# Optimization experiments

Measured on AMD Instinct MI355X. Metric: run time of the kernel, lower is better.

Reference implementation:

```python
import jax, jax.numpy as jnp
import numpy as np

I, H, O = 256, 512, 256  # input_size, hidden_size, output_size
B, S = 4096, 50


def _lstm_cell(x_t, h, c, Wih, Whh, bih, bhh):
    # torch gate order: i, f, g, o
    gates = x_t @ Wih.T + h @ Whh.T + bih + bhh  # [B, 4H]
    i, f, g, o = jnp.split(gates, 4, axis=-1)
    i = jax.nn.sigmoid(i)
    f = jax.nn.sigmoid(f)
    g = jnp.tanh(g)
    o = jax.nn.sigmoid(o)
    c_new = f * c + i * g
    h_new = o * jnp.tanh(c_new)
    return h_new, c_new


def setup_inputs() -> dict:
    key = jax.random.key(0)
    ks = jax.random.split(key, 12)
    s_i = 1.0 / np.sqrt(H)  # torch LSTM/Linear init scale
    u = lambda k, shape: jax.random.uniform(k, shape, jnp.float32, -s_i, s_i)
    return {
        "x": jax.random.normal(ks[0], (B, S, I), jnp.float32),
        "enc_Wih": u(ks[1], (4 * H, I)),
        "enc_Whh": u(ks[2], (4 * H, H)),
        "enc_bih": u(ks[3], (4 * H,)),
        "enc_bhh": u(ks[4], (4 * H,)),
        "dec_Wih": u(ks[5], (4 * H, I)),
        "dec_Whh": u(ks[6], (4 * H, H)),
        "dec_bih": u(ks[7], (4 * H,)),
        "dec_bhh": u(ks[8], (4 * H,)),
        "fc_W": u(ks[9], (O, H)),
        "fc_b": u(ks[10], (O,)),
        "target_seq_length": 20,
    }


def reference(x, enc_Wih, enc_Whh, enc_bih, enc_bhh,
              dec_Wih, dec_Whh, dec_bih, dec_bhh,
              fc_W, fc_b, target_seq_length):
    batch = x.shape[0]
    h0 = jnp.zeros((batch, H), x.dtype)
    c0 = jnp.zeros((batch, H), x.dtype)

    # ---- encoder: scan over time ----
    def enc_step(carry, x_t):
        h, c = carry
        h, c = _lstm_cell(x_t, h, c, enc_Wih, enc_Whh, enc_bih, enc_bhh)
        return (h, c), None

    (h, c), _ = jax.lax.scan(enc_step, (h0, c0), jnp.swapaxes(x, 0, 1))

    dec_in0 = jnp.zeros((batch, I), x.dtype)

    def dec_step(carry, _):
        h, c, inp = carry
        h, c = _lstm_cell(inp, h, c, dec_Wih, dec_Whh, dec_bih, dec_bhh)
        out = h @ fc_W.T + fc_b  # [B, O]
        return (h, c, out), out

    _, outs = jax.lax.scan(dec_step, (h, c, dec_in0), None,
                           length=target_seq_length)
    return jnp.swapaxes(outs, 0, 1)  # [B, T, O]
```

## Files before the change

kernel.cpp:

```cpp
#include <hip/hip_runtime.h>

#define I_SZ 256
#define H_SZ 512
#define O_SZ 256
#define B_SZ 4096
#define S_SZ 50
#define T_SZ 20
#define G4H  2048
#define BH   ((size_t)B_SZ * H_SZ)
#define NB   512

#define PAD 72
#define PAD_H 36

typedef _Float16 half8 __attribute__((ext_vector_type(8)));
typedef float f32x4 __attribute__((ext_vector_type(4)));

__device__ __forceinline__ float sigm(float x) {
    return 1.0f / (1.0f + __expf(-x));
}
__device__ __forceinline__ float tanh_fast(float x) {
    float e = __expf(2.0f * x);
    return 1.0f - 2.0f / (e + 1.0f);
}

#define GLDS(gp, lp) __builtin_amdgcn_global_load_lds(                      \
    (const __attribute__((address_space(1))) void*)(gp),                    \
    (__attribute__((address_space(3))) void*)(lp), 16, 0, 0)

#define MEMFENCE asm volatile("" ::: "memory")

__global__ void k_zeroN(unsigned* p, int n) {
    int i = blockIdx.x * blockDim.x + threadIdx.x;
    if (i < n) p[i] = 0u;
}

__global__ void k_cvt(const float* __restrict__ src, _Float16* __restrict__ dst, int n) {
    int i = blockIdx.x * blockDim.x + threadIdx.x;
    if (i < n) dst[i] = (_Float16)src[i];
}

__global__ void k_bias_combine(const float* __restrict__ a, const float* __restrict__ b,
                               float* __restrict__ dst, int n) {
    int i = blockIdx.x * blockDim.x + threadIdx.x;
    if (i < n) dst[i] = a[i] + b[i];
}

__global__ __launch_bounds__(256) void k_cvt_x(const float* __restrict__ x,
                                               _Float16* __restrict__ xT) {
    size_t idx = ((size_t)blockIdx.x * 256 + threadIdx.x) * 8;
    int i = (int)(idx & 255);
    int s = (int)((idx >> 8) % S_SZ);
    size_t b = idx / (256 * S_SZ);
    float4 v0 = *(const float4*)(x + idx);
    float4 v1 = *(const float4*)(x + idx + 4);
    half8 hv;
    hv[0] = (_Float16)v0.x; hv[1] = (_Float16)v0.y;
    hv[2] = (_Float16)v0.z; hv[3] = (_Float16)v0.w;
    hv[4] = (_Float16)v1.x; hv[5] = (_Float16)v1.y;
    hv[6] = (_Float16)v1.z; hv[7] = (_Float16)v1.w;
    *(half8*)(xT + (((size_t)s * B_SZ + b) * I_SZ + i)) = hv;
}

__global__ void k_wenc(const float* __restrict__ eWih, const float* __restrict__ eWhh,
                       _Float16* __restrict__ Wenc) {
    int idx = blockIdx.x * blockDim.x + threadIdx.x;
    int r = idx / 768, col = idx % 768;
    float v = (col < 256) ? eWih[(size_t)r * 256 + col] : eWhh[(size_t)r * 512 + col - 256];
    Wenc[idx] = (_Float16)v;
}

__global__ __launch_bounds__(256) void k_wd(
    const float* __restrict__ dWhh, const float* __restrict__ dWih,
    const float* __restrict__ fcW, _Float16* __restrict__ Wd)
{
    __shared__ float sA[8][256];
    const int tid = threadIdx.x;
    const int r0 = blockIdx.x * 8;
    {
        int linear = tid * 8;
        int row = linear >> 8, col = linear & 255;
        const float4* p = (const float4*)(dWih + (size_t)(r0 + row) * 256 + col);
        float4 v0 = p[0], v1 = p[1];
        *(float4*)&sA[row][col]     = v0;
        *(float4*)&sA[row][col + 4] = v1;
    }
    __syncthreads();
    float acc[8][2] = {};
    const int k = tid;
    for (int i = 0; i < 256; ++i) {
        float w0 = fcW[(size_t)i * 512 + k];
        float w1 = fcW[(size_t)i * 512 + k + 256];
        #pragma unroll
        for (int rr = 0; rr < 8; ++rr) {
            float a = sA[rr][i];
            acc[rr][0] += a * w0;
            acc[rr][1] += a * w1;
        }
    }
    #pragma unroll
    for (int rr = 0; rr < 8; ++rr) {
        size_t base = (size_t)(r0 + rr) * 512;
        Wd[base + k]       = (_Float16)(dWhh[base + k]       + acc[rr][0]);
        Wd[base + k + 256] = (_Float16)(dWhh[base + k + 256] + acc[rr][1]);
    }
}

__global__ __launch_bounds__(256) void k_bd(
    const float* __restrict__ dWih, const float* __restrict__ fcb,
    const float* __restrict__ db, float* __restrict__ bd)
{
    __shared__ float sf[256];
    const int tid = threadIdx.x;
    sf[tid] = fcb[tid];
    __syncthreads();
    int r = blockIdx.x * 256 + tid;
    float acc = db[r];
    const float* row = dWih + (size_t)r * 256;
    for (int o = 0; o < 256; o += 4) {
        float4 v = *(const float4*)(row + o);
        acc += v.x * sf[o] + v.y * sf[o + 1] + v.z * sf[o + 2] + v.w * sf[o + 3];
    }
    bd[r] = acc;
}

__global__ __launch_bounds__(256, 2) void k_lstm_all(
    const _Float16* __restrict__ xT,
    const _Float16* __restrict__ Wenc,
    const _Float16* __restrict__ dWhh_h,
    const _Float16* __restrict__ Wd,
    const float* __restrict__ eb, const float* __restrict__ db,
    const float* __restrict__ bd,
    _Float16* __restrict__ henc,
    _Float16* __restrict__ hseq,
    unsigned* __restrict__ bar)
{
    __shared__ _Float16 lds[2][2][128 * 64];

    const int tid = threadIdx.x;
    const int xcd = blockIdx.x & 7, slot = blockIdx.x >> 3;
    const int mb = xcd * 4 + (slot >> 4);
    const int jb = slot & 15;
    const int m0 = mb * 128, j0 = jb * 32;
    unsigned* grp = bar + mb * 16;

    const int wv = tid >> 6, lane = tid & 63, lrow = lane & 15, lk8 = (lane >> 4) * 8;
    const int wm = wv >> 1, wn = wv & 1;

    const int colb  = (lane & 7) * 16;
    const int scolh = (colb ^ (((lane >> 3) & 7) << 4)) >> 1;
    const _Float16* wEncQ[4]; const _Float16* wD0Q[4]; const _Float16* wDQ[4];
    const _Float16* xQ[4];
    unsigned aOffQ[4];
    int ldsQ[4];
    #pragma unroll
    for (int q = 0; q < 4; ++q) {
        int r = q * 32 + wv * 8 + (lane >> 3);
        int grow = ((r >> 4) & 3) * H_SZ + j0 + (r >> 6) * 16 + (r & 15);
        wEncQ[q] = Wenc   + (size_t)grow * 768 + scolh;
        wD0Q[q]  = dWhh_h + (size_t)grow * 512 + scolh;
        wDQ[q]   = Wd     + (size_t)grow * 512 + scolh;
        xQ[q]    = xT + (size_t)(m0 + r) * I_SZ + scolh;
        aOffQ[q] = (unsigned)((m0 + r) * H_SZ) + scolh;
        ldsQ[q]  = (q * 256 + wv * 64) * 8;
    }

    float ebj[4], dbj[4], bdj[4];
    #pragma unroll
    for (int nf = 0; nf < 4; ++nf) {
        int col = nf * H_SZ + j0 + wn * 16 + lrow;
        ebj[nf] = eb[col]; dbj[nf] = db[col]; bdj[nf] = bd[col];
    }

    float creg[4][4];

    auto wait_group = [&](unsigned target) {
        MEMFENCE;
        if (tid == 0) {
            while (__hip_atomic_load(grp, __ATOMIC_RELAXED, __HIP_MEMORY_SCOPE_AGENT) < target)
                __builtin_amdgcn_s_sleep(1);
        }
        __builtin_amdgcn_s_barrier();
        MEMFENCE;
    };
    auto arrive = [&]() {
        __syncthreads();
        if (tid == 0)
            __hip_atomic_fetch_add(grp, 1u, __ATOMIC_RELAXED, __HIP_MEMORY_SCOPE_AGENT);
    };

    auto compute = [&](int buf, f32x4 (&acc)[4][4]) {
        #pragma unroll
        for (int kc = 0; kc < 2; ++kc) {
            const int sc = (((kc * 32 + lk8) * 2) ^ ((lrow & 7) << 4)) >> 1;
            half8 a[4], b[4];
            #pragma unroll
            for (int mf = 0; mf < 4; ++mf)
                a[mf] = *(const half8*)&lds[buf][0][(wm * 64 + mf * 16 + lrow) * 64 + sc];
            #pragma unroll
            for (int nf = 0; nf < 4; ++nf)
                b[nf] = *(const half8*)&lds[buf][1][(wn * 64 + nf * 16 + lrow) * 64 + sc];
            #pragma unroll
            for (int mf = 0; mf < 4; ++mf)
                #pragma unroll
                for (int nf = 0; nf < 4; ++nf)
                    acc[mf][nf] = __builtin_amdgcn_mfma_f32_16x16x32_f16(a[mf], b[nf], acc[mf][nf], 0, 0, 0);
        }
    };

    auto epilogue = [&](f32x4 (&acc)[4][4], const float (&bj)[4], _Float16* hout, bool first) {
        _Float16* hsm = &lds[0][0][0];
        const int lc = wn * 16 + lrow;
        #pragma unroll
        for (int mf = 0; mf < 4; ++mf)
            #pragma unroll
            for (int r = 0; r < 4; ++r) {
                int lr = wm * 64 + mf * 16 + (lane >> 4) * 4 + r;
                float gi = acc[mf][0][r] + bj[0];
                float gf = acc[mf][1][r] + bj[1];
                float gg = acc[mf][2][r] + bj[2];
                float go = acc[mf][3][r] + bj[3];
                float cold = first ? 0.0f : creg[mf][r];
                float cn = sigm(gf) * cold + sigm(gi) * tanh_fast(gg);
                creg[mf][r] = cn;
                hsm[lr * PAD_H + lc] = (_Float16)(sigm(go) * tanh_fast(cn));
            }
        __syncthreads();
        int rr = tid >> 3, k = tid & 7;
        #pragma unroll
        for (int q = 0; q < 4; ++q) {
            int r = rr + q * 32;
            unsigned long long v = *(const unsigned long long*)&hsm[r * PAD_H + k * 4];
            unsigned long long* dst =
                (unsigned long long*)(hout + (size_t)(m0 + r) * H_SZ + j0) + k;
            __hip_atomic_store(dst, v, __ATOMIC_RELAXED, __HIP_MEMORY_SCOPE_AGENT);
        }
    };

    {
        f32x4 acc[4][4] = {};
        #pragma unroll
        for (int q = 0; q < 4; ++q) { GLDS(xQ[q], &lds[0][0][ldsQ[q]]); GLDS(wEncQ[q], &lds[0][1][ldsQ[q]]); }
        #pragma unroll
        for (int it = 0; it < 4; ++it) {
            if (it < 3) {
                #pragma unroll
                for (int q = 0; q < 4; ++q) {
                    GLDS(xQ[q] + (it + 1) * 64, &lds[(it + 1) & 1][0][ldsQ[q]]);
                    GLDS(wEncQ[q] + (it + 1) * 64, &lds[(it + 1) & 1][1][ldsQ[q]]);
                }
                asm volatile("s_waitcnt vmcnt(8)" ::: "memory");
            } else {
                asm volatile("s_waitcnt vmcnt(0)" ::: "memory");
            }
            __builtin_amdgcn_s_barrier(); MEMFENCE;
            compute(it & 1, acc);
            MEMFENCE; __builtin_amdgcn_s_barrier(); MEMFENCE;
        }
        epilogue(acc, ebj, henc, true);
        arrive();
    }

    for (int s = 1; s < S_SZ; ++s) {
        const size_t xoff = (size_t)s * B_SZ * I_SZ;
        const _Float16* hin = henc + (size_t)(s - 1) * BH;
        _Float16* hout = (s == S_SZ - 1) ? hseq : henc + (size_t)s * BH;
        f32x4 acc[4][4] = {};
        #pragma unroll
        for (int q = 0; q < 4; ++q) { GLDS(xQ[q] + xoff, &lds[0][0][ldsQ[q]]); GLDS(wEncQ[q], &lds[0][1][ldsQ[q]]); }
        #pragma unroll
        for (int it = 0; it < 12; ++it) {
            if (it < 11) {
                if (it == 3) wait_group((unsigned)s * 16u);
                #pragma unroll
                for (int q = 0; q < 4; ++q) {
                    if (it + 1 < 4) GLDS(xQ[q] + xoff + (it + 1) * 64, &lds[(it + 1) & 1][0][ldsQ[q]]);
                    else            GLDS(hin + aOffQ[q] + (it - 3) * 64, &lds[(it + 1) & 1][0][ldsQ[q]]);
                    GLDS(wEncQ[q] + (it + 1) * 64, &lds[(it + 1) & 1][1][ldsQ[q]]);
                }
                asm volatile("s_waitcnt vmcnt(8)" ::: "memory");
            } else {
                asm volatile("s_waitcnt vmcnt(0)" ::: "memory");
            }
            __builtin_amdgcn_s_barrier(); MEMFENCE;
            compute(it & 1, acc);
            MEMFENCE; __builtin_amdgcn_s_barrier(); MEMFENCE;
        }
        epilogue(acc, ebj, hout, false);
        arrive();
    }

    for (int t = 0; t < T_SZ; ++t) {
        const _Float16* hin = hseq + (size_t)t * BH;
        _Float16* hout = hseq + (size_t)(t + 1) * BH;
        const _Float16* wq[4];
        float bj[4];
        #pragma unroll
        for (int q = 0; q < 4; ++q) wq[q] = t ? wDQ[q] : wD0Q[q];
        #pragma unroll
        for (int nf = 0; nf < 4; ++nf) bj[nf] = t ? bdj[nf] : dbj[nf];

        wait_group((unsigned)(S_SZ + t) * 16u);
        f32x4 acc[4][4] = {};
        #pragma unroll
        for (int q = 0; q < 4; ++q) { GLDS(hin + aOffQ[q], &lds[0][0][ldsQ[q]]); GLDS(wq[q], &lds[0][1][ldsQ[q]]); }
        #pragma unroll
        for (int it = 0; it < 8; ++it) {
            if (it < 7) {
                #pragma unroll
                for (int q = 0; q < 4; ++q) {
                    GLDS(hin + aOffQ[q] + (it + 1) * 64, &lds[(it + 1) & 1][0][ldsQ[q]]);
                    GLDS(wq[q] + (it + 1) * 64, &lds[(it + 1) & 1][1][ldsQ[q]]);
                }
                asm volatile("s_waitcnt vmcnt(8)" ::: "memory");
            } else {
                asm volatile("s_waitcnt vmcnt(0)" ::: "memory");
            }
            __builtin_amdgcn_s_barrier(); MEMFENCE;
            compute(it & 1, acc);
            MEMFENCE; __builtin_amdgcn_s_barrier(); MEMFENCE;
        }
        epilogue(acc, bj, hout, false);
        if (t != T_SZ - 1) arrive();
    }
}

__global__ __launch_bounds__(256) void k_fc(
    const _Float16* __restrict__ hseq1,
    const _Float16* __restrict__ W,
    const float* __restrict__ bias,
    float* __restrict__ out)
{
    __shared__ _Float16 Asm[128][PAD];
    __shared__ _Float16 Bsm[128][PAD];

    const int tid = threadIdx.x;
    const int m0 = blockIdx.x * 128;
    const int t  = blockIdx.y;
    const int n0 = blockIdx.z * 128;
    const int wv = tid >> 6, lane = tid & 63, lrow = lane & 15, lk = (lane >> 4) * 8;
    const int wm = wv >> 1, wn = wv & 1;

    f32x4 acc[4][4] = {};

    const int srow = tid >> 3, skc = (tid & 7) * 8;
    const _Float16* A = hseq1 + (size_t)t * BH;

    for (int k0 = 0; k0 < H_SZ; k0 += 64) {
        __syncthreads();
        #pragma unroll
        for (int q = 0; q < 4; ++q) {
            int r = srow + q * 32;
            *(half8*)&Asm[r][skc] = *(const half8*)(A + (size_t)(m0 + r) * H_SZ + k0 + skc);
        }
        #pragma unroll
        for (int q = 0; q < 4; ++q) {
            int rr = srow + q * 32;
            *(half8*)&Bsm[rr][skc] = *(const half8*)(W + (size_t)(n0 + rr) * H_SZ + k0 + skc);
        }
        __syncthreads();
        #pragma unroll
        for (int kc = 0; kc < 64; kc += 32) {
            half8 a[4], b[4];
            #pragma unroll
            for (int mf = 0; mf < 4; ++mf) a[mf] = *(const half8*)&Asm[wm * 64 + mf * 16 + lrow][kc + lk];
            #pragma unroll
            for (int nf = 0; nf < 4; ++nf) b[nf] = *(const half8*)&Bsm[wn * 64 + nf * 16 + lrow][kc + lk];
            #pragma unroll
            for (int mf = 0; mf < 4; ++mf)
                #pragma unroll
                for (int nf = 0; nf < 4; ++nf)
                    acc[mf][nf] = __builtin_amdgcn_mfma_f32_16x16x32_f16(a[mf], b[nf], acc[mf][nf], 0, 0, 0);
        }
    }

    #pragma unroll
    for (int mf = 0; mf < 4; ++mf)
        #pragma unroll
        for (int nf = 0; nf < 4; ++nf) {
            int o = n0 + wn * 64 + nf * 16 + lrow;
            float bv = bias[o];
            #pragma unroll
            for (int r = 0; r < 4; ++r) {
                int m = m0 + wm * 64 + mf * 16 + (lane >> 4) * 4 + r;
                out[(size_t)m * (T_SZ * O_SZ) + (size_t)t * O_SZ + o] = acc[mf][nf][r] + bv;
            }
        }
}

extern "C" void kernel_launch(void* const* d_in, const int* in_sizes, int n_in,
                              void* d_out, int out_size, void* d_ws, size_t ws_size,
                              hipStream_t stream) {
    (void)in_sizes; (void)n_in; (void)out_size; (void)ws_size;

    const float* x    = (const float*)d_in[0];
    const float* eWih = (const float*)d_in[1];
    const float* eWhh = (const float*)d_in[2];
    const float* ebih = (const float*)d_in[3];
    const float* ebhh = (const float*)d_in[4];
    const float* dWih = (const float*)d_in[5];
    const float* dWhh = (const float*)d_in[6];
    const float* dbih = (const float*)d_in[7];
    const float* dbhh = (const float*)d_in[8];
    const float* fcW  = (const float*)d_in[9];
    const float* fcb  = (const float*)d_in[10];
    float* out = (float*)d_out;
    char* ws = (char*)d_ws;

    size_t off = 0;
    auto alloc = [&](size_t bytes) -> void* {
        void* p = ws + off;
        off += (bytes + 255) & ~(size_t)255;
        return p;
    };
    _Float16* xT     = (_Float16*)alloc((size_t)S_SZ * B_SZ * I_SZ * 2);
    _Float16* Wenc   = (_Float16*)alloc((size_t)G4H * (I_SZ + H_SZ) * 2);
    _Float16* dWhh_h = (_Float16*)alloc((size_t)G4H * H_SZ * 2);
    _Float16* Wd     = (_Float16*)alloc((size_t)G4H * H_SZ * 2);
    _Float16* fcW_h  = (_Float16*)alloc((size_t)O_SZ * H_SZ * 2);
    float*    eb     = (float*)alloc(G4H * 4);
    float*    db     = (float*)alloc(G4H * 4);
    float*    bd     = (float*)alloc(G4H * 4);
    _Float16* henc   = (_Float16*)alloc((size_t)(S_SZ - 1) * BH * 2);
    _Float16* hseq   = (_Float16*)alloc((size_t)(T_SZ + 1) * BH * 2);
    unsigned* bar    = (unsigned*)alloc(32 * 16 * 4);

    const int nWhh = G4H * H_SZ;
    const int nFc  = O_SZ * H_SZ;
    const size_t nX = (size_t)B_SZ * S_SZ * I_SZ;

    k_zeroN<<<2, 256, 0, stream>>>(bar, 32 * 16);
    k_cvt_x<<<(int)(nX / 8 / 256), 256, 0, stream>>>(x, xT);
    k_wenc<<<(G4H * 768) / 256, 256, 0, stream>>>(eWih, eWhh, Wenc);
    k_cvt<<<(nWhh + 255) / 256, 256, 0, stream>>>(dWhh, dWhh_h, nWhh);
    k_cvt<<<(nFc + 255) / 256, 256, 0, stream>>>(fcW, fcW_h, nFc);
    k_bias_combine<<<8, 256, 0, stream>>>(ebih, ebhh, eb, G4H);
    k_bias_combine<<<8, 256, 0, stream>>>(dbih, dbhh, db, G4H);
    k_wd<<<256, 256, 0, stream>>>(dWhh, dWih, fcW, Wd);
    k_bd<<<8, 256, 0, stream>>>(dWih, fcb, db, bd);

    k_lstm_all<<<NB, 256, 0, stream>>>(xT, Wenc, dWhh_h, Wd, eb, db, bd,
                                       henc, hseq, bar);

    k_fc<<<dim3(B_SZ / 128, T_SZ, O_SZ / 128), 256, 0, stream>>>(
        hseq + BH, fcW_h, fcb, out);
}
```

Measured before the change: 1.271 ms.

## Load A operand straight to registers and ring-buffer weights in four LDS stages

The recurrent step is restructured so that activation tiles (x and h) are loaded from global memory directly into registers, double-buffered, instead of being staged through LDS. Weight tiles go into a four-slot LDS ring prefetched two iterations ahead, which removes the second block barrier in each K-iteration. The group-arrive signal now fires early in the next step, after its weight loads are issued, so cross-block synchronisation overlaps with prefetch. The cost is more register pressure and less efficient global access for A, and the tighter synchronisation raises the risk of LDS hazards.

```diff
diff --git a/kernel.cpp b/kernel.cpp
--- a/kernel.cpp
+++ b/kernel.cpp
@@ -15,6 +15,8 @@
 
 typedef _Float16 half8 __attribute__((ext_vector_type(8)));
 typedef float f32x4 __attribute__((ext_vector_type(4)));
+
+template<int N> struct IC { static constexpr int value = N; };
 
 __device__ __forceinline__ float sigm(float x) {
     return 1.0f / (1.0f + __expf(-x));
@@ -135,7 +137,7 @@
     _Float16* __restrict__ hseq,
     unsigned* __restrict__ bar)
 {
-    __shared__ _Float16 lds[2][2][128 * 64];
+    __shared__ _Float16 Bs[4][8192];
 
     const int tid = threadIdx.x;
     const int xcd = blockIdx.x & 7, slot = blockIdx.x >> 3;
@@ -147,22 +149,24 @@
     const int wv = tid >> 6, lane = tid & 63, lrow = lane & 15, lk8 = (lane >> 4) * 8;
     const int wm = wv >> 1, wn = wv & 1;
 
-    const int colb  = (lane & 7) * 16;
-    const int scolh = (colb ^ (((lane >> 3) & 7) << 4)) >> 1;
-    const _Float16* wEncQ[4]; const _Float16* wD0Q[4]; const _Float16* wDQ[4];
-    const _Float16* xQ[4];
-    unsigned aOffQ[4];
+    const int scolh = (((lane & 7) * 16) ^ (((lane >> 3) & 7) << 4)) >> 1;
+    unsigned woffE[4], woffD[4];
     int ldsQ[4];
     #pragma unroll
     for (int q = 0; q < 4; ++q) {
         int r = q * 32 + wv * 8 + (lane >> 3);
-        int grow = ((r >> 4) & 3) * H_SZ + j0 + (r >> 6) * 16 + (r & 15);
-        wEncQ[q] = Wenc   + (size_t)grow * 768 + scolh;
-        wD0Q[q]  = dWhh_h + (size_t)grow * 512 + scolh;
-        wDQ[q]   = Wd     + (size_t)grow * 512 + scolh;
-        xQ[q]    = xT + (size_t)(m0 + r) * I_SZ + scolh;
-        aOffQ[q] = (unsigned)((m0 + r) * H_SZ) + scolh;
+        unsigned grow = ((r >> 4) & 3) * H_SZ + j0 + (r >> 6) * 16 + (r & 15);
+        woffE[q] = grow * 768u + scolh;
+        woffD[q] = grow * 512u + scolh;
         ldsQ[q]  = (q * 256 + wv * 64) * 8;
+    }
+
+    unsigned aoffX[4], aoffH[4];
+    #pragma unroll
+    for (int mf = 0; mf < 4; ++mf) {
+        unsigned row = (unsigned)(m0 + wm * 64 + mf * 16 + lrow);
+        aoffX[mf] = row * (unsigned)I_SZ + (unsigned)lk8;
+        aoffH[mf] = row * (unsigned)H_SZ + (unsigned)lk8;
     }
 
     float ebj[4], dbj[4], bdj[4];
@@ -183,33 +187,85 @@
         __builtin_amdgcn_s_barrier();
         MEMFENCE;
     };
-    auto arrive = [&]() {
-        __syncthreads();
-        if (tid == 0)
-            __hip_atomic_fetch_add(grp, 1u, __ATOMIC_RELAXED, __HIP_MEMORY_SCOPE_AGENT);
-    };
-
-    auto compute = [&](int buf, f32x4 (&acc)[4][4]) {
-        #pragma unroll
-        for (int kc = 0; kc < 2; ++kc) {
-            const int sc = (((kc * 32 + lk8) * 2) ^ ((lrow & 7) << 4)) >> 1;
-            half8 a[4], b[4];
-            #pragma unroll
-            for (int mf = 0; mf < 4; ++mf)
-                a[mf] = *(const half8*)&lds[buf][0][(wm * 64 + mf * 16 + lrow) * 64 + sc];
-            #pragma unroll
-            for (int nf = 0; nf < 4; ++nf)
-                b[nf] = *(const half8*)&lds[buf][1][(wn * 64 + nf * 16 + lrow) * 64 + sc];
+
+    auto run_step = [&](auto NITERc, auto NXc, bool first, bool sig, unsigned wtarget,
+                        const _Float16* xs, const _Float16* hin,
+                        const _Float16* wb, const unsigned* woff,
+                        const float* bj, _Float16* hout) {
+        constexpr int NITER = decltype(NITERc)::value;
+        constexpr int NX    = decltype(NXc)::value;
+
+        half8 ar[2][4][2];
+        f32x4 acc[4][4];
+        #pragma unroll
+        for (int mf = 0; mf < 4; ++mf)
+            #pragma unroll
+            for (int nf = 0; nf < 4; ++nf) {
+                f32x4 z = {0.f, 0.f, 0.f, 0.f};
+                acc[mf][nf] = z;
+            }
+
+        auto loadA = [&](int it2) {
             #pragma unroll
             for (int mf = 0; mf < 4; ++mf)
                 #pragma unroll
+                for (int kc = 0; kc < 2; ++kc)
+                    ar[it2 & 1][mf][kc] = (it2 < NX)
+                        ? *(const half8*)(xs + aoffX[mf] + it2 * 64 + kc * 32)
+                        : *(const half8*)(hin + aoffH[mf] + (it2 - NX) * 64 + kc * 32);
+        };
+        auto stageB = [&](int it2) {
+            #pragma unroll
+            for (int q = 0; q < 4; ++q)
+                GLDS(wb + woff[q] + it2 * 64, &Bs[it2 & 3][ldsQ[q]]);
+        };
+
+        if (NX == 0) {
+            stageB(0); stageB(1);
+            asm volatile("s_waitcnt vmcnt(8)" ::: "memory");
+            __builtin_amdgcn_s_barrier(); MEMFENCE;
+            if (sig && tid == 0)
+                __hip_atomic_fetch_add(grp, 1u, __ATOMIC_RELAXED, __HIP_MEMORY_SCOPE_AGENT);
+            wait_group(wtarget);
+            loadA(0);
+        } else {
+            loadA(0); stageB(0); stageB(1);
+            if (sig) {
+                asm volatile("s_waitcnt vmcnt(16)" ::: "memory");
+                __builtin_amdgcn_s_barrier(); MEMFENCE;
+                if (tid == 0)
+                    __hip_atomic_fetch_add(grp, 1u, __ATOMIC_RELAXED, __HIP_MEMORY_SCOPE_AGENT);
+            }
+        }
+
+        #pragma unroll
+        for (int it = 0; it < NITER; ++it) {
+            if (NX > 0 && NITER > NX && it == NX - 1) wait_group(wtarget);
+            if (it + 1 < NITER) loadA(it + 1);
+            if (it + 2 < NITER) stageB(it + 2);
+            if (NX == 0 && it == 0)   { asm volatile("s_waitcnt vmcnt(12)" ::: "memory"); }
+            else if (it + 2 < NITER)  { asm volatile("s_waitcnt vmcnt(16)" ::: "memory"); }
+            else if (it + 1 < NITER)  { asm volatile("s_waitcnt vmcnt(12)" ::: "memory"); }
+            else                      { asm volatile("s_waitcnt vmcnt(0)"  ::: "memory"); }
+            __builtin_amdgcn_s_barrier(); MEMFENCE;
+            #pragma unroll
+            for (int kc = 0; kc < 2; ++kc) {
+                const int sc = (((kc * 32 + lk8) * 2) ^ ((lrow & 7) << 4)) >> 1;
+                half8 b[4];
+                #pragma unroll
                 for (int nf = 0; nf < 4; ++nf)
-                    acc[mf][nf] = __builtin_amdgcn_mfma_f32_16x16x32_f16(a[mf], b[nf], acc[mf][nf], 0, 0, 0);
-        }
-    };
-
-    auto epilogue = [&](f32x4 (&acc)[4][4], const float (&bj)[4], _Float16* hout, bool first) {
-        _Float16* hsm = &lds[0][0][0];
+                    b[nf] = *(const half8*)&Bs[it & 3][(wn * 64 + nf * 16 + lrow) * 64 + sc];
+                #pragma unroll
+                for (int mf = 0; mf < 4; ++mf)
+                    #pragma unroll
+                    for (int nf = 0; nf < 4; ++nf)
+                        acc[mf][nf] = __builtin_amdgcn_mfma_f32_16x16x32_f16(
+                            ar[it & 1][mf][kc], b[nf], acc[mf][nf], 0, 0, 0);
+            }
+            MEMFENCE;
+        }
+
+        _Float16* hsm = &Bs[2][0];
         const int lc = wn * 16 + lrow;
         #pragma unroll
         for (int mf = 0; mf < 4; ++mf)
@@ -226,102 +282,34 @@
                 hsm[lr * PAD_H + lc] = (_Float16)(sigm(go) * tanh_fast(cn));
             }
         __syncthreads();
-        int rr = tid >> 3, k = tid & 7;
-        #pragma unroll
-        for (int q = 0; q < 4; ++q) {
-            int r = rr + q * 32;
-            unsigned long long v = *(const unsigned long long*)&hsm[r * PAD_H + k * 4];
-            unsigned long long* dst =
-                (unsigned long long*)(hout + (size_t)(m0 + r) * H_SZ + j0) + k;
-            __hip_atomic_store(dst, v, __ATOMIC_RELAXED, __HIP_MEMORY_SCOPE_AGENT);
+        {
+            int rr = tid >> 3, k = tid & 7;
+            #pragma unroll
+            for (int q = 0; q < 4; ++q) {
+                int r = rr + q * 32;
+                unsigned long long v = *(const unsigned long long*)&hsm[r * PAD_H + k * 4];
+                unsigned long long* dst =
+                    (unsigned long long*)(hout + (size_t)(m0 + r) * H_SZ + j0) + k;
+                __hip_atomic_store(dst, v, __ATOMIC_RELAXED, __HIP_MEMORY_SCOPE_AGENT);
+            }
         }
     };
 
-    {
-        f32x4 acc[4][4] = {};
-        #pragma unroll
-        for (int q = 0; q < 4; ++q) { GLDS(xQ[q], &lds[0][0][ldsQ[q]]); GLDS(wEncQ[q], &lds[0][1][ldsQ[q]]); }
-        #pragma unroll
-        for (int it = 0; it < 4; ++it) {
-            if (it < 3) {
-                #pragma unroll
-                for (int q = 0; q < 4; ++q) {
-                    GLDS(xQ[q] + (it + 1) * 64, &lds[(it + 1) & 1][0][ldsQ[q]]);
-                    GLDS(wEncQ[q] + (it + 1) * 64, &lds[(it + 1) & 1][1][ldsQ[q]]);
-                }
-                asm volatile("s_waitcnt vmcnt(8)" ::: "memory");
-            } else {
-                asm volatile("s_waitcnt vmcnt(0)" ::: "memory");
-            }
-            __builtin_amdgcn_s_barrier(); MEMFENCE;
-            compute(it & 1, acc);
-            MEMFENCE; __builtin_amdgcn_s_barrier(); MEMFENCE;
-        }
-        epilogue(acc, ebj, henc, true);
-        arrive();
-    }
+    run_step(IC<4>{}, IC<4>{}, true, false, 0u,
+             xT, henc, Wenc, woffE, ebj, henc);
 
     for (int s = 1; s < S_SZ; ++s) {
-        const size_t xoff = (size_t)s * B_SZ * I_SZ;
-        const _Float16* hin = henc + (size_t)(s - 1) * BH;
-        _Float16* hout = (s == S_SZ - 1) ? hseq : henc + (size_t)s * BH;
-        f32x4 acc[4][4] = {};
-        #pragma unroll
-        for (int q = 0; q < 4; ++q) { GLDS(xQ[q] + xoff, &lds[0][0][ldsQ[q]]); GLDS(wEncQ[q], &lds[0][1][ldsQ[q]]); }
-        #pragma unroll
-        for (int it = 0; it < 12; ++it) {
-            if (it < 11) {
-                if (it == 3) wait_group((unsigned)s * 16u);
-                #pragma unroll
-                for (int q = 0; q < 4; ++q) {
-                    if (it + 1 < 4) GLDS(xQ[q] + xoff + (it + 1) * 64, &lds[(it + 1) & 1][0][ldsQ[q]]);
-                    else            GLDS(hin + aOffQ[q] + (it - 3) * 64, &lds[(it + 1) & 1][0][ldsQ[q]]);
-                    GLDS(wEncQ[q] + (it + 1) * 64, &lds[(it + 1) & 1][1][ldsQ[q]]);
-                }
-                asm volatile("s_waitcnt vmcnt(8)" ::: "memory");
-            } else {
-                asm volatile("s_waitcnt vmcnt(0)" ::: "memory");
-            }
-            __builtin_amdgcn_s_barrier(); MEMFENCE;
-            compute(it & 1, acc);
-            MEMFENCE; __builtin_amdgcn_s_barrier(); MEMFENCE;
-        }
-        epilogue(acc, ebj, hout, false);
-        arrive();
+        run_step(IC<12>{}, IC<4>{}, false, true, (unsigned)s * 16u,
+                 xT + (size_t)s * B_SZ * I_SZ,
+                 henc + (size_t)(s - 1) * BH, Wenc, woffE, ebj,
+                 (s == S_SZ - 1) ? hseq : henc + (size_t)s * BH);
     }
 
     for (int t = 0; t < T_SZ; ++t) {
-        const _Float16* hin = hseq + (size_t)t * BH;
-        _Float16* hout = hseq + (size_t)(t + 1) * BH;
-        const _Float16* wq[4];
-        float bj[4];
-        #pragma unroll
-        for (int q = 0; q < 4; ++q) wq[q] = t ? wDQ[q] : wD0Q[q];
-        #pragma unroll
-        for (int nf = 0; nf < 4; ++nf) bj[nf] = t ? bdj[nf] : dbj[nf];
-
-        wait_group((unsigned)(S_SZ + t) * 16u);
-        f32x4 acc[4][4] = {};
-        #pragma unroll
-        for (int q = 0; q < 4; ++q) { GLDS(hin + aOffQ[q], &lds[0][0][ldsQ[q]]); GLDS(wq[q], &lds[0][1][ldsQ[q]]); }
-        #pragma unroll
-        for (int it = 0; it < 8; ++it) {
-            if (it < 7) {
-                #pragma unroll
-                for (int q = 0; q < 4; ++q) {
-                    GLDS(hin + aOffQ[q] + (it + 1) * 64, &lds[(it + 1) & 1][0][ldsQ[q]]);
-                    GLDS(wq[q] + (it + 1) * 64, &lds[(it + 1) & 1][1][ldsQ[q]]);
-                }
-                asm volatile("s_waitcnt vmcnt(8)" ::: "memory");
-            } else {
-                asm volatile("s_waitcnt vmcnt(0)" ::: "memory");
-            }
-            __builtin_amdgcn_s_barrier(); MEMFENCE;
-            compute(it & 1, acc);
-            MEMFENCE; __builtin_amdgcn_s_barrier(); MEMFENCE;
-        }
-        epilogue(acc, bj, hout, false);
-        if (t != T_SZ - 1) arrive();
+        run_step(IC<8>{}, IC<0>{}, false, true, (unsigned)(S_SZ + t) * 16u,
+                 henc, hseq + (size_t)t * BH,
+                 t ? Wd : dWhh_h, woffD, t ? bdj : dbj,
+                 hseq + (size_t)(t + 1) * BH);
     }
 }
 
```

After: 2.285 ms. +79.8%, slower.
